# Kernel tuning notes

Measured on AMD Instinct MI355X. Metric: run time of the kernel, lower is better.

The kernel has to match this reference:

```python
import jax, jax.numpy as jnp
import numpy as np

N, E = 50000, 800000
IN_DIM, E_DIM, OUT_DIM, H = 128, 32, 16, 4
NEG_SLOPE = 0.2


def setup_inputs() -> dict:
    key = jax.random.key(0)
    ks = jax.random.split(key, 9)
    return {
        "feat": jax.random.normal(ks[0], (N, IN_DIM), jnp.float32),
        "edge_attr": jax.random.normal(ks[1], (E, E_DIM), jnp.float32),
        "src": jax.random.randint(ks[2], (E,), 0, N),
        "dst": jax.random.randint(ks[3], (E,), 0, N),
        "W_fc": jax.random.normal(ks[4], (OUT_DIM * H, IN_DIM), jnp.float32) * 0.1,
        "W_edge": jax.random.normal(ks[5], (OUT_DIM * H, E_DIM), jnp.float32) * 0.1,
        "attn_h": jax.random.normal(ks[6], (1, H, OUT_DIM), jnp.float32) * 0.1,
        "attn_t": jax.random.normal(ks[7], (1, H, OUT_DIM), jnp.float32) * 0.1,
        "attn_e": jax.random.normal(ks[8], (1, H, OUT_DIM), jnp.float32) * 0.1,
        "bias": jnp.zeros((1, H, OUT_DIM), jnp.float32),
    }


def reference(feat, edge_attr, src, dst, W_fc, W_edge, attn_h, attn_t, attn_e, bias):
    n = feat.shape[0]
    # node / edge projections
    feat_ = (feat @ W_fc.T).reshape(n, H, OUT_DIM)          # [N,H,D]
    eh = (feat_ * attn_h).sum(-1)                            # [N,H]
    et = (feat_ * attn_t).sum(-1)                            # [N,H]
    feat_e = (edge_attr @ W_edge.T).reshape(-1, H, OUT_DIM)  # [E,H,D]
    ee = (feat_e * attn_e).sum(-1)                           # [E,H]
    # per-edge attention logits: u_add_e then e_add_v, then leaky relu
    e = eh[src] + ee + et[dst]                               # [E,H]
    e = jnp.where(e > 0, e, NEG_SLOPE * e)
    # edge softmax grouped by destination node
    e_max = jax.ops.segment_max(e, dst, num_segments=n)      # [N,H]
    e_max = jnp.where(jnp.isfinite(e_max), e_max, 0.0)
    a = jnp.exp(e - e_max[dst])                              # [E,H]
    a_sum = jax.ops.segment_sum(a, dst, num_segments=n)      # [N,H]
    a = a / jnp.where(a_sum[dst] > 0, a_sum[dst], 1.0)
    # u_mul_e + sum aggregation
    msg = feat_[src] * a[:, :, None]                         # [E,H,D]
    rst = jax.ops.segment_sum(msg, dst, num_segments=n)      # [N,H,D]
    rst = rst + bias
    return rst.reshape(n, H * OUT_DIM)                       # concat_out
```

## Files before the change

### kernel.cpp

```cpp
#include <hip/hip_runtime.h>

#define NN 50000
#define EE 800000
#define IND 128
#define EDD 32
#define ODD 16
#define NH 4
#define HD 64
#define NEG_SLOPE 0.2f
#define NBLK ((NN + 255) / 256)

typedef float  f32x4 __attribute__((ext_vector_type(4)));
typedef int    i32x2 __attribute__((ext_vector_type(2)));
typedef int    i32x4 __attribute__((ext_vector_type(4)));
typedef _Float16 f16x8 __attribute__((ext_vector_type(8)));

union h2i { int i; _Float16 h[2]; };

__global__ __launch_bounds__(256)
void k_init_prep(int* __restrict__ deg, const float* __restrict__ W_fc,
                 const float* __restrict__ W_edge, const float* __restrict__ attn_e,
                 float* __restrict__ Wt, float* __restrict__ w_ee) {
    int i = blockIdx.x * 256 + threadIdx.x;
    if (i < NN) deg[i] = 0;
    if (i < HD * IND) {
        int k = i >> 6, j = i & 63;
        Wt[i] = W_fc[j * IND + k];
    }
    if (i < NH * EDD) {
        int h = i >> 5, k = i & 31;
        float s = 0.f;
        for (int d = 0; d < ODD; ++d)
            s += W_edge[(h * ODD + d) * EDD + k] * attn_e[h * ODD + d];
        w_ee[i] = s;
    }
}

__global__ __launch_bounds__(256)
void k_node(const float* __restrict__ feat, const float* __restrict__ Wt,
            const float* __restrict__ attn_h, const float* __restrict__ attn_t,
            _Float16* __restrict__ feat_h, float2* __restrict__ eh2,
            float2* __restrict__ et2) {
    int n = blockIdx.x * 256 + threadIdx.x;
    int hf = blockIdx.y;
    if (n >= NN) return;
    const int jbase = hf * 32;
    f32x4 row[32];
    const f32x4* fr4 = (const f32x4*)(feat + (long)n * IND);
#pragma unroll
    for (int q = 0; q < 32; ++q) row[q] = __builtin_nontemporal_load(fr4 + q);
    asm volatile("" ::: "memory");
    float acc[32];
#pragma unroll
    for (int j = 0; j < 32; ++j) acc[j] = 0.f;
#pragma unroll
    for (int k0 = 0; k0 < 32; ++k0) {
        float f[4] = {row[k0][0], row[k0][1], row[k0][2], row[k0][3]};
#pragma unroll
        for (int kk = 0; kk < 4; ++kk) {
            const float* w = Wt + (k0 * 4 + kk) * HD + jbase;
#pragma unroll
            for (int j = 0; j < 32; ++j) acc[j] += f[kk] * w[j];
        }
    }
    f16x8* d8 = (f16x8*)(feat_h + (long)n * HD + jbase);
#pragma unroll
    for (int q = 0; q < 4; ++q) {
        f16x8 v;
#pragma unroll
        for (int j = 0; j < 8; ++j) v[j] = (_Float16)acc[q * 8 + j];
        d8[q] = v;
    }
    float sh[2], st[2];
#pragma unroll
    for (int hh = 0; hh < 2; ++hh) {
        sh[hh] = 0.f; st[hh] = 0.f;
        int hg = hf * 2 + hh;
#pragma unroll
        for (int d = 0; d < ODD; ++d) {
            float av = acc[hh * ODD + d];
            sh[hh] += av * attn_h[hg * ODD + d];
            st[hh] += av * attn_t[hg * ODD + d];
        }
    }
    eh2[n * 2 + hf] = make_float2(sh[0], sh[1]);
    et2[n * 2 + hf] = make_float2(st[0], st[1]);
}

__global__ __launch_bounds__(256)
void k_hist(const int* __restrict__ dst, int* __restrict__ deg, int* __restrict__ rank) {
    int e = blockIdx.x * 256 + threadIdx.x;
    if (e < EE) rank[e] = atomicAdd(&deg[dst[e]], 1);
}

__global__ __launch_bounds__(256)
void k_scan1(const int* __restrict__ deg, int* __restrict__ offs, int* __restrict__ part) {
    __shared__ int s[256];
    int t = threadIdx.x, i = blockIdx.x * 256 + t;
    int v = (i < NN) ? deg[i] : 0;
    s[t] = v;
    __syncthreads();
#pragma unroll
    for (int o = 1; o < 256; o <<= 1) {
        int u = (t >= o) ? s[t - o] : 0;
        __syncthreads();
        if (t >= o) s[t] += u;
        __syncthreads();
    }
    if (i < NN) offs[i] = s[t] - v;
    if (t == 255) part[blockIdx.x] = s[255];
}

__global__ __launch_bounds__(256)
void k_scan2(int* __restrict__ part) {
    __shared__ int s[256];
    int t = threadIdx.x;
    int v = (t < NBLK) ? part[t] : 0;
    s[t] = v;
    __syncthreads();
#pragma unroll
    for (int o = 1; o < 256; o <<= 1) {
        int u = (t >= o) ? s[t - o] : 0;
        __syncthreads();
        if (t >= o) s[t] += u;
        __syncthreads();
    }
    if (t < NBLK) part[t] = s[t] - v;
}

__global__ __launch_bounds__(256)
void k_scan3(int* __restrict__ offs, const int* __restrict__ part) {
    int i = blockIdx.x * 256 + threadIdx.x;
    if (i < NN) offs[i] += part[i >> 8];
}

__global__ __launch_bounds__(256)
void k_logit2(const float* __restrict__ edge_attr, const int* __restrict__ dst,
              const int* __restrict__ src, const float* __restrict__ w_ee,
              const int* __restrict__ offs, const int* __restrict__ rank,
              i32x4* __restrict__ rec4) {
    int t = blockIdx.x * 256 + threadIdx.x;
    int e0 = t * 2;
    if (e0 >= EE) return;
    i32x2 d2 = *(const i32x2*)(dst + e0);
    i32x2 r2 = *(const i32x2*)(rank + e0);
    i32x2 s2 = *(const i32x2*)(src + e0);
    int o0 = offs[d2[0]], o1 = offs[d2[1]];
    const f32x4* ea = (const f32x4*)(edge_attr + (long)e0 * EDD);
    f32x4 r[16];
#pragma unroll
    for (int c = 0; c < 16; ++c) r[c] = ea[c];
    asm volatile("" ::: "memory");
    const float* f0 = (const float*)&r[0];
    const float* f1 = (const float*)&r[8];
    float z0[NH], z1[NH];
#pragma unroll
    for (int h = 0; h < NH; ++h) {
        float a = 0.f, b = 0.f;
#pragma unroll
        for (int k = 0; k < EDD; ++k) {
            float w = w_ee[h * EDD + k];
            a += f0[k] * w;
            b += f1[k] * w;
        }
        z0[h] = a; z1[h] = b;
    }
    h2i p01, p23, q01, q23;
    p01.h[0] = (_Float16)z0[0]; p01.h[1] = (_Float16)z0[1];
    p23.h[0] = (_Float16)z0[2]; p23.h[1] = (_Float16)z0[3];
    q01.h[0] = (_Float16)z1[0]; q01.h[1] = (_Float16)z1[1];
    q23.h[0] = (_Float16)z1[2]; q23.h[1] = (_Float16)z1[3];
    i32x4 rc0 = {s2[0], p01.i, p23.i, 0};
    i32x4 rc1 = {s2[1], q01.i, q23.i, 0};
    rec4[o0 + r2[0]] = rc0;
    rec4[o1 + r2[1]] = rc1;
}

__global__ __launch_bounds__(256)
void k_reduce(const int* __restrict__ offs, const int* __restrict__ deg,
              const i32x4* __restrict__ rec4,
              const float* __restrict__ eh, const float* __restrict__ et,
              const _Float16* __restrict__ feat_h, const float* __restrict__ bias,
              float* __restrict__ out) {
    int wid = (blockIdx.x * 256 + threadIdx.x) >> 6;
    int lane = threadIdx.x & 63;
    if (wid >= NN) return;
    int start = __builtin_amdgcn_readfirstlane(offs[wid]);
    int dn    = __builtin_amdgcn_readfirstlane(deg[wid]);
    int h = lane >> 4;
    int q = lane & 15;
    float et_h = et[(long)wid * 4 + h];
    float acc = 0.f, l = 0.f;

    for (int c0 = 0; c0 < dn; c0 += 16) {
        int rem = dn - c0; if (rem > 16) rem = 16;
        int qq = (q < rem) ? q : (rem - 1);
        i32x4 r = rec4[start + c0 + qq];
        int   s_q = r.x;
        h2i u; u.i = (h & 2) ? r.z : r.y;
        float z = (float)u.h[h & 1];
        float x = z + eh[(long)s_q * 4 + h] + et_h;
        x = x > 0.f ? x : NEG_SLOPE * x;
        float a_q = (q < rem) ? __expf(x) : 0.f;
        float f[16];
#pragma unroll
        for (int i = 0; i < 16; ++i) {
            int si = __shfl(s_q, i);
            f[i] = (float)feat_h[(long)si * HD + lane];
        }
#pragma unroll
        for (int i = 0; i < 16; ++i) {
            float ai = __shfl(a_q, (lane & 48) + i);
            l += ai;
            acc += ai * f[i];
        }
    }
    float res = (l > 0.f) ? acc / l : 0.f;
    __builtin_nontemporal_store(res + bias[lane], &out[(long)wid * HD + lane]);
}

extern "C" void kernel_launch(void* const* d_in, const int* in_sizes, int n_in,
                              void* d_out, int out_size, void* d_ws, size_t ws_size,
                              hipStream_t stream) {
    const float* feat      = (const float*)d_in[0];
    const float* edge_attr = (const float*)d_in[1];
    const int*   src       = (const int*)d_in[2];
    const int*   dst       = (const int*)d_in[3];
    const float* W_fc      = (const float*)d_in[4];
    const float* W_edge    = (const float*)d_in[5];
    const float* attn_h    = (const float*)d_in[6];
    const float* attn_t    = (const float*)d_in[7];
    const float* attn_e    = (const float*)d_in[8];
    const float* bias      = (const float*)d_in[9];
    float* out             = (float*)d_out;

    float* ws        = (float*)d_ws;
    i32x4*  rec4     = (i32x4*)ws;
    float4* eh4      = (float4*)(rec4 + EE);
    float4* et4      = eh4 + NN;
    _Float16* feat_h = (_Float16*)(et4 + NN);
    float*  Wt       = (float*)(feat_h + (long)NN * HD);
    float*  w_ee     = Wt + HD * IND;
    int*    rank     = (int*)(w_ee + NH * EDD);
    int*    deg      = rank + EE;
    int*    offs     = deg + NN;
    int*    part     = offs + NN;

    k_init_prep<<<NBLK, 256, 0, stream>>>(deg, W_fc, W_edge, attn_e, Wt, w_ee);
    dim3 ngrid(NBLK, 2);
    k_node<<<ngrid, 256, 0, stream>>>(feat, Wt, attn_h, attn_t, feat_h,
                                      (float2*)eh4, (float2*)et4);
    k_hist<<<(EE + 255) / 256, 256, 0, stream>>>(dst, deg, rank);
    k_scan1<<<NBLK, 256, 0, stream>>>(deg, offs, part);
    k_scan2<<<1, 256, 0, stream>>>(part);
    k_scan3<<<NBLK, 256, 0, stream>>>(offs, part);
    k_logit2<<<(EE / 2 + 255) / 256, 256, 0, stream>>>(edge_attr, dst, src, w_ee,
                                                       offs, rank, rec4);
    k_reduce<<<(NN * 64 + 255) / 256, 256, 0, stream>>>(offs, deg, rec4,
                                                        (const float*)eh4,
                                                        (const float*)et4,
                                                        feat_h, bias, out);
}
```

Baseline: 348.1 us.

## Coalesce edge_attr loads in logit kernel using octet-cooperative dot products with shuffles

The edge-logit kernel is rewritten so each wave handles 64 edges. Groups of eight lanes cooperatively load each edge's 32-float attribute row with fully coalesced 16-byte loads, reduce the per-head dot products with xor shuffles, and broadcast src/dst/rank via shuffles before one lane writes the record. Before, each thread read two whole rows with strided per-thread loads. This replaces uncoalesced traffic with coalesced traffic at the cost of extra shuffle instructions and idle lanes during the store. The node kernel's feat loads also switch from nontemporal to normal loads.

```diff
diff --git a/kernel.cpp b/kernel.cpp
--- a/kernel.cpp
+++ b/kernel.cpp
@@ -48,7 +48,7 @@
     f32x4 row[32];
     const f32x4* fr4 = (const f32x4*)(feat + (long)n * IND);
 #pragma unroll
-    for (int q = 0; q < 32; ++q) row[q] = __builtin_nontemporal_load(fr4 + q);
+    for (int q = 0; q < 32; ++q) row[q] = fr4[q];
     asm volatile("" ::: "memory");
     float acc[32];
 #pragma unroll
@@ -135,45 +135,54 @@
 }
 
 __global__ __launch_bounds__(256)
-void k_logit2(const float* __restrict__ edge_attr, const int* __restrict__ dst,
+void k_logit8(const float* __restrict__ edge_attr, const int* __restrict__ dst,
               const int* __restrict__ src, const float* __restrict__ w_ee,
               const int* __restrict__ offs, const int* __restrict__ rank,
               i32x4* __restrict__ rec4) {
-    int t = blockIdx.x * 256 + threadIdx.x;
-    int e0 = t * 2;
-    if (e0 >= EE) return;
-    i32x2 d2 = *(const i32x2*)(dst + e0);
-    i32x2 r2 = *(const i32x2*)(rank + e0);
-    i32x2 s2 = *(const i32x2*)(src + e0);
-    int o0 = offs[d2[0]], o1 = offs[d2[1]];
-    const f32x4* ea = (const f32x4*)(edge_attr + (long)e0 * EDD);
-    f32x4 r[16];
-#pragma unroll
-    for (int c = 0; c < 16; ++c) r[c] = ea[c];
+    int tid = threadIdx.x;
+    int wave = tid >> 6, lane = tid & 63;
+    long wbase = (long)blockIdx.x * 256 + wave * 64;
+    int dv = dst[wbase + lane];
+    int rv = rank[wbase + lane];
+    int sv = src[wbase + lane];
+    int oct = lane >> 3;
+    int ol  = lane & 7;
+    float wr[NH][4];
+#pragma unroll
+    for (int h = 0; h < NH; ++h) {
+        f32x4 wv = *(const f32x4*)(w_ee + h * EDD + ol * 4);
+        wr[h][0] = wv[0]; wr[h][1] = wv[1]; wr[h][2] = wv[2]; wr[h][3] = wv[3];
+    }
+    f32x4 u[8];
+    const f32x4* ea = (const f32x4*)(edge_attr + wbase * EDD);
+#pragma unroll
+    for (int p = 0; p < 8; ++p) u[p] = ea[p * 64 + lane];
     asm volatile("" ::: "memory");
-    const float* f0 = (const float*)&r[0];
-    const float* f1 = (const float*)&r[8];
-    float z0[NH], z1[NH];
-#pragma unroll
-    for (int h = 0; h < NH; ++h) {
-        float a = 0.f, b = 0.f;
-#pragma unroll
-        for (int k = 0; k < EDD; ++k) {
-            float w = w_ee[h * EDD + k];
-            a += f0[k] * w;
-            b += f1[k] * w;
-        }
-        z0[h] = a; z1[h] = b;
-    }
-    h2i p01, p23, q01, q23;
-    p01.h[0] = (_Float16)z0[0]; p01.h[1] = (_Float16)z0[1];
-    p23.h[0] = (_Float16)z0[2]; p23.h[1] = (_Float16)z0[3];
-    q01.h[0] = (_Float16)z1[0]; q01.h[1] = (_Float16)z1[1];
-    q23.h[0] = (_Float16)z1[2]; q23.h[1] = (_Float16)z1[3];
-    i32x4 rc0 = {s2[0], p01.i, p23.i, 0};
-    i32x4 rc1 = {s2[1], q01.i, q23.i, 0};
-    rec4[o0 + r2[0]] = rc0;
-    rec4[o1 + r2[1]] = rc1;
+#pragma unroll
+    for (int p = 0; p < 8; ++p) {
+        float z[NH];
+#pragma unroll
+        for (int h = 0; h < NH; ++h)
+            z[h] = u[p][0] * wr[h][0] + u[p][1] * wr[h][1]
+                 + u[p][2] * wr[h][2] + u[p][3] * wr[h][3];
+#pragma unroll
+        for (int h = 0; h < NH; ++h) {
+            z[h] += __shfl_xor(z[h], 1);
+            z[h] += __shfl_xor(z[h], 2);
+            z[h] += __shfl_xor(z[h], 4);
+        }
+        int ei   = p * 8 + oct;
+        int lsrc = __shfl(sv, ei);
+        int ld   = __shfl(dv, ei);
+        int lr   = __shfl(rv, ei);
+        if (ol == 0) {
+            h2i z01, z23;
+            z01.h[0] = (_Float16)z[0]; z01.h[1] = (_Float16)z[1];
+            z23.h[0] = (_Float16)z[2]; z23.h[1] = (_Float16)z[3];
+            i32x4 rc = {lsrc, z01.i, z23.i, 0};
+            rec4[offs[ld] + lr] = rc;
+        }
+    }
 }
 
 __global__ __launch_bounds__(256)
@@ -254,8 +263,8 @@
     k_scan1<<<NBLK, 256, 0, stream>>>(deg, offs, part);
     k_scan2<<<1, 256, 0, stream>>>(part);
     k_scan3<<<NBLK, 256, 0, stream>>>(offs, part);
-    k_logit2<<<(EE / 2 + 255) / 256, 256, 0, stream>>>(edge_attr, dst, src, w_ee,
-                                                       offs, rank, rec4);
+    k_logit8<<<EE / 256, 256, 0, stream>>>(edge_attr, dst, src, w_ee,
+                                           offs, rank, rec4);
     k_reduce<<<(NN * 64 + 255) / 256, 256, 0, stream>>>(offs, deg, rec4,
                                                         (const float*)eh4,
                                                         (const float*)et4,
```

Result: faster. 331.2 us (-4.8%).
